# Kernel tuning notes

Hardware: AMD Instinct MI355X
Metric: run time of the kernel (lower is better)

## Reference

```python
import jax, jax.numpy as jnp
import numpy as np
import math

D_MODEL = 1024
NUM_HEADS = 16
D_K = D_MODEL // NUM_HEADS  # 64
THETA = 10000.0
B, S = 2, 2048


def setup_inputs() -> dict:
    key = jax.random.key(0)
    kx, kq, kk, kv, ko = jax.random.split(key, 5)
    sigma = (2.0 / (D_MODEL + D_MODEL)) ** 0.5
    return {
        "x": jax.random.normal(kx, (B, S, D_MODEL), dtype=jnp.float32),
        "Wq": jax.random.normal(kq, (D_MODEL, D_MODEL), dtype=jnp.float32) * sigma,
        "Wk": jax.random.normal(kk, (D_MODEL, D_MODEL), dtype=jnp.float32) * sigma,
        "Wv": jax.random.normal(kv, (D_MODEL, D_MODEL), dtype=jnp.float32) * sigma,
        "Wo": jax.random.normal(ko, (D_MODEL, D_MODEL), dtype=jnp.float32) * sigma,
        "token_positions": jnp.arange(S, dtype=jnp.int32),
    }


def _rope(x, token_positions):
    # x: [..., seq, d_k]; rotate interleaved even/odd pairs.
    half = x.shape[-1] // 2
    freq = jnp.power(THETA, -jnp.arange(0, x.shape[-1], 2, dtype=jnp.float32) / x.shape[-1])  # [half]
    angles = token_positions[:, None].astype(jnp.float32) * freq[None, :]  # [seq, half]
    cos, sin = jnp.cos(angles), jnp.sin(angles)
    x1 = x[..., 0::2]
    x2 = x[..., 1::2]
    out = jnp.stack([x1 * cos - x2 * sin, x1 * sin + x2 * cos], axis=-1)  # [..., seq, half, 2]
    return out.reshape(x.shape)


def reference(x, Wq, Wk, Wv, Wo, token_positions):
    Bb, Ss, Dm = x.shape
    H, Dk = NUM_HEADS, D_K
    # Linear: y = x @ W.T ; split as (n head) -> heads first
    def heads(y):
        return y.reshape(Bb, Ss, H, Dk).transpose(0, 2, 1, 3)  # [B,H,S,Dk]
    Q = heads(x @ Wq.T)
    K = heads(x @ Wk.T)
    V = heads(x @ Wv.T)
    Q = _rope(Q, token_positions)
    K = _rope(K, token_positions)
    scores = jnp.einsum("bhqd,bhkd->bhqk", Q, K) / math.sqrt(Dk)  # [B,H,S,S]
    causal = jnp.tril(jnp.ones((Ss, Ss), dtype=bool))
    scores = jnp.where(causal, scores, -jnp.inf)
    # original casts to fp64 for softmax; numerically-stable fp32 softmax here
    probs = jax.nn.softmax(scores, axis=-1)
    attn = jnp.einsum("bhqk,bhkd->bhqd", probs, V)  # [B,H,S,Dk]
    attn = attn.transpose(0, 2, 1, 3).reshape(Bb, Ss, Dm)
    return attn @ Wo.T
```

## Files before the change

### kernel.cpp

```cpp
#include <hip/hip_runtime.h>
#include <hip/hip_bf16.h>
#include <math.h>

typedef __bf16 bf16_t;
typedef __attribute__((ext_vector_type(8))) __bf16 bf16x8;
typedef __attribute__((ext_vector_type(4))) __bf16 bf16x4;
typedef __attribute__((ext_vector_type(4))) float f32x4;

#define B_DIM 2
#define S_DIM 2048
#define H_DIM 16
#define DK 64
#define DM 1024
#define KDIM 1024

#define MFMA(a, b, c) __builtin_amdgcn_mfma_f32_16x16x32_bf16((a), (b), (c), 0, 0, 0)

__device__ __forceinline__ void gload_lds16(const bf16_t* g, bf16_t* l) {
    __builtin_amdgcn_global_load_lds(
        (const __attribute__((address_space(1))) void*)g,
        (__attribute__((address_space(3))) void*)l, 16, 0, 0);
}

__global__ void cvt_all(const float* __restrict__ x,
                        const float* __restrict__ wq, const float* __restrict__ wk,
                        const float* __restrict__ wv, const float* __restrict__ wo,
                        bf16_t* __restrict__ xb,
                        bf16_t* __restrict__ wqb, bf16_t* __restrict__ wkb,
                        bf16_t* __restrict__ wvb, bf16_t* __restrict__ wob) {
    const long NX = (long)B_DIM * S_DIM * DM;
    const long i = ((long)blockIdx.x * 256 + threadIdx.x) * 4;
    const float* s; bf16_t* d; long off;
    if (i < NX) { s = x; d = xb; off = i; }
    else {
        const long j = i - NX;
        const int wsel = (int)(j >> 20);
        off = j & ((1L << 20) - 1);
        switch (wsel) {
            case 0: s = wq; d = wqb; break;
            case 1: s = wk; d = wkb; break;
            case 2: s = wv; d = wvb; break;
            default: s = wo; d = wob; break;
        }
    }
    float4 v = *reinterpret_cast<const float4*>(s + off);
    bf16x4 o;
    o[0] = (__bf16)v.x; o[1] = (__bf16)v.y; o[2] = (__bf16)v.z; o[3] = (__bf16)v.w;
    *reinterpret_cast<bf16x4*>(d + off) = o;
}

template <int MODE>
__global__ __launch_bounds__(256)
void gemm_bt(const bf16_t* __restrict__ A,
             const bf16_t* __restrict__ B0,
             const bf16_t* __restrict__ B1,
             const bf16_t* __restrict__ B2,
             bf16_t* __restrict__ outQ,
             bf16_t* __restrict__ outK,
             bf16_t* __restrict__ outVt,
             float* __restrict__ outF,
             const int* __restrict__ pos) {
    constexpr int CP = 136;
    constexpr int SELEMS = (MODE == 0) ? (128 * CP) : 16384;
    __shared__ bf16_t smem[SELEMS];
    bf16_t* As = smem;
    bf16_t* Bs = smem + 8192;
    bf16_t* Cs = smem;

    const int t = threadIdx.x;
    const int z = blockIdx.z;
    const bf16_t* Bm = (MODE == 0) ? (z == 0 ? B0 : (z == 1 ? B1 : B2)) : B0;

    const int m0 = blockIdx.x * 128;
    const int n0 = blockIdx.y * 128;
    const int lane = t & 63;
    const int w = t >> 6;
    const int wr = w >> 1;
    const int wc = w & 1;

    f32x4 acc[4][4] = {};

    const bf16_t* Ag = A + (size_t)m0 * KDIM;
    const bf16_t* Bg = Bm + (size_t)n0 * KDIM;

    const int rr = lane & 15;
    const int ko = (lane >> 4) * 8;

    int rI[4], cI[4];
#pragma unroll
    for (int c = 0; c < 4; ++c) {
        const int i = t + c * 256;
        rI[c] = i >> 3;
        cI[c] = ((i & 7) ^ (rI[c] & 7)) * 8;
    }

    for (int k0 = 0; k0 < KDIM; k0 += 64) {
#pragma unroll
        for (int c = 0; c < 4; ++c) {
            const int i = t + c * 256;
            gload_lds16(Ag + (size_t)rI[c] * KDIM + k0 + cI[c], &As[i * 8]);
        }
#pragma unroll
        for (int c = 0; c < 4; ++c) {
            const int i = t + c * 256;
            gload_lds16(Bg + (size_t)rI[c] * KDIM + k0 + cI[c], &Bs[i * 8]);
        }
        __syncthreads();

        bf16x8 af[2][4], bfr[2][4];
#pragma unroll
        for (int kk = 0; kk < 2; ++kk) {
#pragma unroll
            for (int m = 0; m < 4; ++m) {
                const int r = wr * 64 + m * 16 + rr;
                af[kk][m] = *reinterpret_cast<const bf16x8*>(
                    &As[r * 64 + ((kk * 32 + ko) ^ ((r & 7) * 8))]);
            }
#pragma unroll
            for (int n = 0; n < 4; ++n) {
                const int r = wc * 64 + n * 16 + rr;
                bfr[kk][n] = *reinterpret_cast<const bf16x8*>(
                    &Bs[r * 64 + ((kk * 32 + ko) ^ ((r & 7) * 8))]);
            }
        }
        __builtin_amdgcn_s_setprio(1);
#pragma unroll
        for (int kk = 0; kk < 2; ++kk)
#pragma unroll
            for (int m = 0; m < 4; ++m)
#pragma unroll
                for (int n = 0; n < 4; ++n)
                    acc[m][n] = MFMA(af[kk][m], bfr[kk][n], acc[m][n]);
        __builtin_amdgcn_s_setprio(0);
        __syncthreads();
    }

    const int rlb = wr * 64 + (lane >> 4) * 4;
    const int clb = wc * 64 + (lane & 15);

    if (MODE == 0) {
        if (z < 2) {
#pragma unroll
            for (int m = 0; m < 4; ++m)
#pragma unroll
                for (int n = 0; n < 4; ++n)
#pragma unroll
                    for (int j = 0; j < 4; ++j)
                        Cs[(rlb + m * 16 + j) * CP + clb + n * 16] = (__bf16)acc[m][n][j];
            __syncthreads();

            bf16_t* dst = (z == 0) ? outQ : outK;
            const int dch = t & 7;
            const int srow = t >> 3;
            float fr[4];
#pragma unroll
            for (int i = 0; i < 4; ++i)
                fr[i] = exp2f((float)(dch * 4 + i) * -0.4152410118609203f);
#pragma unroll
            for (int p = 0; p < 4; ++p) {
                const int s_loc = p * 32 + srow;
                const int gm = m0 + s_loc;
                const int bb = gm >> 11, sg = gm & (S_DIM - 1);
                const float pv = (float)pos[sg];
                float csv[4], snv[4];
#pragma unroll
                for (int i = 0; i < 4; ++i) {
                    const float a = pv * fr[i];
                    csv[i] = cosf(a); snv[i] = sinf(a);
                }
#pragma unroll
                for (int hc = 0; hc < 2; ++hc) {
                    const bf16x8 vv = *reinterpret_cast<const bf16x8*>(
                        &Cs[s_loc * CP + hc * 64 + dch * 8]);
                    bf16x8 ov;
#pragma unroll
                    for (int i = 0; i < 4; ++i) {
                        const float v0 = (float)vv[2 * i], v1 = (float)vv[2 * i + 1];
                        ov[2 * i]     = (__bf16)(v0 * csv[i] - v1 * snv[i]);
                        ov[2 * i + 1] = (__bf16)(v0 * snv[i] + v1 * csv[i]);
                    }
                    const int h = (n0 >> 6) + hc;
                    *reinterpret_cast<bf16x8*>(
                        &dst[((size_t)(bb * H_DIM + h) * S_DIM + sg) * 64 + dch * 8]) = ov;
                }
            }
        } else {
#pragma unroll
            for (int m = 0; m < 4; ++m)
#pragma unroll
                for (int n = 0; n < 4; ++n) {
                    const int cl = clb + n * 16;
                    bf16x4 v4;
#pragma unroll
                    for (int j = 0; j < 4; ++j) v4[j] = (__bf16)acc[m][n][j];
                    *reinterpret_cast<bf16x4*>(&Cs[cl * CP + rlb + m * 16]) = v4;
                }
            __syncthreads();

            const int cl = t >> 1, sh = t & 1;
            const int cg = n0 + cl, h = cg >> 6, d = cg & 63;
            const int bb = m0 >> 11, s0g = m0 & (S_DIM - 1);
            bf16_t* vdst = &outVt[((size_t)(bb * H_DIM + h) * DK + d) * S_DIM + s0g + sh * 64];
#pragma unroll
            for (int i = 0; i < 8; ++i)
                *reinterpret_cast<bf16x8*>(&vdst[i * 8]) =
                    *reinterpret_cast<const bf16x8*>(&Cs[cl * CP + sh * 64 + i * 8]);
        }
    } else {
        const int rbase = m0 + rlb;
        const int cbase = n0 + clb;
#pragma unroll
        for (int m = 0; m < 4; ++m)
#pragma unroll
            for (int n = 0; n < 4; ++n)
#pragma unroll
                for (int j = 0; j < 4; ++j)
                    outF[(size_t)(rbase + m * 16 + j) * DM + cbase + n * 16] = acc[m][n][j];
    }
}

__global__ __launch_bounds__(256)
void attn_kernel(const bf16_t* __restrict__ Q, const bf16_t* __restrict__ Kg,
                 const bf16_t* __restrict__ Vt, bf16_t* __restrict__ O) {
    constexpr int PSTR = 72;
    __shared__ bf16_t Ks[2][64 * 64];
    __shared__ bf16_t Vs[2][64 * 64];
    __shared__ bf16_t P_lds[4][2][16 * PSTR];

    const int t = threadIdx.x;
    const int lane = t & 63;
    const int w = t >> 6;
    const int bh = blockIdx.x >> 4;
    const int qi = blockIdx.x & 15;
    const int qbH = 31 - qi, qbL = qi;
    const int q0H = qbH * 64 + w * 16;
    const int q0L = qbL * 64 + w * 16;
    const int b = bh >> 4, h = bh & 15;
    const int rr = lane & 15;
    const int hi = lane >> 4;

    const bf16_t* Kbh = Kg + (size_t)bh * S_DIM * DK;
    const bf16_t* Vbh = Vt + (size_t)bh * DK * S_DIM;
    bf16_t* PwH = P_lds[w][0];
    bf16_t* PwL = P_lds[w][1];

    const int i0 = t, i1 = t + 256;
    const int r0 = i0 >> 3, c0 = ((i0 & 7) ^ (r0 & 7)) * 8;
    const int r1 = i1 >> 3, c1 = ((i1 & 7) ^ (r1 & 7)) * 8;

    const float QSCALE = 0.18033688011112042f;
    const bf16_t* QpH = Q + ((size_t)bh * S_DIM + q0H) * DK;
    const bf16_t* QpL = Q + ((size_t)bh * S_DIM + q0L) * DK;
    bf16x8 qfH[2], qfL[2];
    qfH[0] = *reinterpret_cast<const bf16x8*>(&QpH[rr * DK + hi * 8]);
    qfH[1] = *reinterpret_cast<const bf16x8*>(&QpH[rr * DK + 32 + hi * 8]);
    qfL[0] = *reinterpret_cast<const bf16x8*>(&QpL[rr * DK + hi * 8]);
    qfL[1] = *reinterpret_cast<const bf16x8*>(&QpL[rr * DK + 32 + hi * 8]);
#pragma unroll
    for (int i = 0; i < 8; ++i) {
        qfH[0][i] = (__bf16)((float)qfH[0][i] * QSCALE);
        qfH[1][i] = (__bf16)((float)qfH[1][i] * QSCALE);
        qfL[0][i] = (__bf16)((float)qfL[0][i] * QSCALE);
        qfL[1][i] = (__bf16)((float)qfL[1][i] * QSCALE);
    }

    bf16x8 ones;
#pragma unroll
    for (int i = 0; i < 8; ++i) ones[i] = (__bf16)1.0f;

    f32x4 oH[4] = {}, oL[4] = {};
    f32x4 laH = {}, laL = {};
    float mH = -INFINITY, mL = -INFINITY;

    const int ntH = qbH + 1;

    gload_lds16(Kbh + (size_t)r0 * DK + c0, &Ks[0][i0 * 8]);
    gload_lds16(Kbh + (size_t)r1 * DK + c1, &Ks[0][i1 * 8]);
    gload_lds16(Vbh + (size_t)r0 * S_DIM + c0, &Vs[0][i0 * 8]);
    gload_lds16(Vbh + (size_t)r1 * S_DIM + c1, &Vs[0][i1 * 8]);
    __syncthreads();

    for (int tt = 0; tt < ntH; ++tt) {
        const int cur = tt & 1;
        const int kv0 = tt * 64;
        const bool doL = (tt <= qbL);

        if (tt + 1 < ntH) {
            const int kv1 = kv0 + 64;
            bf16_t* Kn = Ks[cur ^ 1];
            bf16_t* Vn = Vs[cur ^ 1];
            gload_lds16(Kbh + (size_t)(kv1 + r0) * DK + c0, &Kn[i0 * 8]);
            gload_lds16(Kbh + (size_t)(kv1 + r1) * DK + c1, &Kn[i1 * 8]);
            gload_lds16(Vbh + (size_t)r0 * S_DIM + kv1 + c0, &Vn[i0 * 8]);
            gload_lds16(Vbh + (size_t)r1 * S_DIM + kv1 + c1, &Vn[i1 * 8]);
        }
        const bf16_t* Kc = Ks[cur];
        const bf16_t* Vc = Vs[cur];

        f32x4 sH[4] = {}, sL[4] = {};
        __builtin_amdgcn_s_setprio(1);
#pragma unroll
        for (int t16 = 0; t16 < 4; ++t16) {
            const int r = t16 * 16 + rr;
            const int sw = (r & 7) * 8;
            bf16x8 kf0 = *reinterpret_cast<const bf16x8*>(&Kc[r * 64 + ((hi * 8) ^ sw)]);
            bf16x8 kf1 = *reinterpret_cast<const bf16x8*>(&Kc[r * 64 + ((32 + hi * 8) ^ sw)]);
            sH[t16] = MFMA(kf0, qfH[0], sH[t16]);
            sH[t16] = MFMA(kf1, qfH[1], sH[t16]);
            if (doL) {
                sL[t16] = MFMA(kf0, qfL[0], sL[t16]);
                sL[t16] = MFMA(kf1, qfL[1], sL[t16]);
            }
        }
        __builtin_amdgcn_s_setprio(0);

        if (tt == qbH) {
            const int qg = q0H + rr;
#pragma unroll
            for (int t16 = 0; t16 < 4; ++t16)
#pragma unroll
                for (int j = 0; j < 4; ++j)
                    if (kv0 + t16 * 16 + hi * 4 + j > qg) sH[t16][j] = -INFINITY;
        }
        if (tt == qbL) {
            const int qg = q0L + rr;
#pragma unroll
            for (int t16 = 0; t16 < 4; ++t16)
#pragma unroll
                for (int j = 0; j < 4; ++j)
                    if (kv0 + t16 * 16 + hi * 4 + j > qg) sL[t16][j] = -INFINITY;
        }

        {
            f32x4 mv = sH[0];
#pragma unroll
            for (int t16 = 1; t16 < 4; ++t16) {
                mv[0] = fmaxf(mv[0], sH[t16][0]); mv[1] = fmaxf(mv[1], sH[t16][1]);
                mv[2] = fmaxf(mv[2], sH[t16][2]); mv[3] = fmaxf(mv[3], sH[t16][3]);
            }
            const float mloc = fmaxf(fmaxf(mv[0], mv[1]), fmaxf(mv[2], mv[3]));
            if (__any(mloc - mH > 8.0f)) {
                float mf = fmaxf(mloc, __shfl_xor(mloc, 16));
                mf = fmaxf(mf, __shfl_xor(mf, 32));
                const float mnew = fmaxf(mH, mf);
                const float scale = exp2f(mH - mnew);
#pragma unroll
                for (int i = 0; i < 4; ++i) laH[i] *= scale;
#pragma unroll
                for (int db = 0; db < 4; ++db)
#pragma unroll
                    for (int j = 0; j < 4; ++j) oH[db][j] *= scale;
                mH = mnew;
            }
#pragma unroll
            for (int t16 = 0; t16 < 4; ++t16) {
                bf16x4 pb;
#pragma unroll
                for (int j = 0; j < 4; ++j) pb[j] = (__bf16)exp2f(sH[t16][j] - mH);
                *reinterpret_cast<bf16x4*>(&PwH[rr * PSTR + t16 * 16 + hi * 4]) = pb;
            }
        }
        if (doL) {
            f32x4 mv = sL[0];
#pragma unroll
            for (int t16 = 1; t16 < 4; ++t16) {
                mv[0] = fmaxf(mv[0], sL[t16][0]); mv[1] = fmaxf(mv[1], sL[t16][1]);
                mv[2] = fmaxf(mv[2], sL[t16][2]); mv[3] = fmaxf(mv[3], sL[t16][3]);
            }
            const float mloc = fmaxf(fmaxf(mv[0], mv[1]), fmaxf(mv[2], mv[3]));
            if (__any(mloc - mL > 8.0f)) {
                float mf = fmaxf(mloc, __shfl_xor(mloc, 16));
                mf = fmaxf(mf, __shfl_xor(mf, 32));
                const float mnew = fmaxf(mL, mf);
                const float scale = exp2f(mL - mnew);
#pragma unroll
                for (int i = 0; i < 4; ++i) laL[i] *= scale;
#pragma unroll
                for (int db = 0; db < 4; ++db)
#pragma unroll
                    for (int j = 0; j < 4; ++j) oL[db][j] *= scale;
                mL = mnew;
            }
#pragma unroll
            for (int t16 = 0; t16 < 4; ++t16) {
                bf16x4 pb;
#pragma unroll
                for (int j = 0; j < 4; ++j) pb[j] = (__bf16)exp2f(sL[t16][j] - mL);
                *reinterpret_cast<bf16x4*>(&PwL[rr * PSTR + t16 * 16 + hi * 4]) = pb;
            }
        }

        bf16x8 pH0 = *reinterpret_cast<const bf16x8*>(&PwH[rr * PSTR + hi * 8]);
        bf16x8 pH1 = *reinterpret_cast<const bf16x8*>(&PwH[rr * PSTR + 32 + hi * 8]);
        bf16x8 pL0, pL1;
        if (doL) {
            pL0 = *reinterpret_cast<const bf16x8*>(&PwL[rr * PSTR + hi * 8]);
            pL1 = *reinterpret_cast<const bf16x8*>(&PwL[rr * PSTR + 32 + hi * 8]);
        }
        __builtin_amdgcn_s_setprio(1);
        laH = MFMA(ones, pH0, laH);
        laH = MFMA(ones, pH1, laH);
        if (doL) {
            laL = MFMA(ones, pL0, laL);
            laL = MFMA(ones, pL1, laL);
        }
#pragma unroll
        for (int db = 0; db < 4; ++db) {
            const int vr = db * 16 + rr;
            const int sw = (vr & 7) * 8;
            bf16x8 vf0 = *reinterpret_cast<const bf16x8*>(&Vc[vr * 64 + ((hi * 8) ^ sw)]);
            bf16x8 vf1 = *reinterpret_cast<const bf16x8*>(&Vc[vr * 64 + ((32 + hi * 8) ^ sw)]);
            oH[db] = MFMA(vf0, pH0, oH[db]);
            oH[db] = MFMA(vf1, pH1, oH[db]);
            if (doL) {
                oL[db] = MFMA(vf0, pL0, oL[db]);
                oL[db] = MFMA(vf1, pL1, oL[db]);
            }
        }
        __builtin_amdgcn_s_setprio(0);

        __syncthreads();
    }

    {
        const float linv = 1.0f / laH[0];
#pragma unroll
        for (int db = 0; db < 4; ++db) {
            bf16x4 ov;
#pragma unroll
            for (int j = 0; j < 4; ++j) ov[j] = (__bf16)(oH[db][j] * linv);
            *reinterpret_cast<bf16x4*>(
                &O[((size_t)(b * S_DIM + q0H + rr)) * DM + h * DK + db * 16 + hi * 4]) = ov;
        }
    }
    {
        const float linv = 1.0f / laL[0];
#pragma unroll
        for (int db = 0; db < 4; ++db) {
            bf16x4 ov;
#pragma unroll
            for (int j = 0; j < 4; ++j) ov[j] = (__bf16)(oL[db][j] * linv);
            *reinterpret_cast<bf16x4*>(
                &O[((size_t)(b * S_DIM + q0L + rr)) * DM + h * DK + db * 16 + hi * 4]) = ov;
        }
    }
}

extern "C" void kernel_launch(void* const* d_in, const int* in_sizes, int n_in,
                              void* d_out, int out_size, void* d_ws, size_t ws_size,
                              hipStream_t stream) {
    const float* x  = (const float*)d_in[0];
    const float* Wq = (const float*)d_in[1];
    const float* Wk = (const float*)d_in[2];
    const float* Wv = (const float*)d_in[3];
    const float* Wo = (const float*)d_in[4];
    const int* pos  = (const int*)d_in[5];
    float* out = (float*)d_out;

    char* ws = (char*)d_ws;
    bf16_t* xb  = (bf16_t*)(ws);
    bf16_t* Wqb = (bf16_t*)(ws + (8u << 20));
    bf16_t* Wkb = (bf16_t*)(ws + (10u << 20));
    bf16_t* Wvb = (bf16_t*)(ws + (12u << 20));
    bf16_t* Wob = (bf16_t*)(ws + (14u << 20));
    bf16_t* Qb  = (bf16_t*)(ws + (16u << 20));
    bf16_t* Kb  = (bf16_t*)(ws + (24u << 20));
    bf16_t* Vtb = (bf16_t*)(ws + (32u << 20));
    bf16_t* Ab  = (bf16_t*)(ws);

    const int NX = B_DIM * S_DIM * DM;
    const int NW = DM * DM;
    const int NTOT = NX + 4 * NW;

    cvt_all<<<NTOT / 1024, 256, 0, stream>>>(x, Wq, Wk, Wv, Wo,
                                             xb, Wqb, Wkb, Wvb, Wob);

    gemm_bt<0><<<dim3(32, 8, 3), 256, 0, stream>>>(xb, Wqb, Wkb, Wvb,
                                                   Qb, Kb, Vtb, nullptr, pos);

    attn_kernel<<<B_DIM * H_DIM * 16, 256, 0, stream>>>(Qb, Kb, Vtb, Ab);

    gemm_bt<1><<<dim3(32, 8, 1), 256, 0, stream>>>(Ab, Wob, nullptr, nullptr,
                                                   nullptr, nullptr, nullptr, out, pos);
}
```

Baseline: 129.8 us.

## Split paired high/low query blocks across separate waves in 512-thread attention blocks

Each attention block now runs 8 waves: waves 0-3 handle the high causal query block and waves 4-7 handle the low one, sharing the same K/V tiles in LDS. Before, each of 4 waves processed both query blocks. Each wave now keeps one set of accumulators, which cuts register pressure and allows more waves per CU for latency hiding. The trade-off is that waves on the low block sit idle at the barriers once their causal range ends, and each K/V tile is now loaded by 512 threads instead of 256.

```diff
diff --git a/kernel.cpp b/kernel.cpp
--- a/kernel.cpp
+++ b/kernel.cpp
@@ -219,13 +219,13 @@
     }
 }
 
-__global__ __launch_bounds__(256)
+__global__ __launch_bounds__(512, 4)
 void attn_kernel(const bf16_t* __restrict__ Q, const bf16_t* __restrict__ Kg,
                  const bf16_t* __restrict__ Vt, bf16_t* __restrict__ O) {
     constexpr int PSTR = 72;
     __shared__ bf16_t Ks[2][64 * 64];
     __shared__ bf16_t Vs[2][64 * 64];
-    __shared__ bf16_t P_lds[4][2][16 * PSTR];
+    __shared__ bf16_t P_lds[8][16 * PSTR];
 
     const int t = threadIdx.x;
     const int lane = t & 63;
@@ -233,216 +233,134 @@
     const int bh = blockIdx.x >> 4;
     const int qi = blockIdx.x & 15;
     const int qbH = 31 - qi, qbL = qi;
-    const int q0H = qbH * 64 + w * 16;
-    const int q0L = qbL * 64 + w * 16;
+    const int qbC = (w < 4) ? qbH : qbL;
+    const int q0 = qbC * 64 + (w & 3) * 16;
     const int b = bh >> 4, h = bh & 15;
     const int rr = lane & 15;
     const int hi = lane >> 4;
 
     const bf16_t* Kbh = Kg + (size_t)bh * S_DIM * DK;
     const bf16_t* Vbh = Vt + (size_t)bh * DK * S_DIM;
-    bf16_t* PwH = P_lds[w][0];
-    bf16_t* PwL = P_lds[w][1];
-
-    const int i0 = t, i1 = t + 256;
-    const int r0 = i0 >> 3, c0 = ((i0 & 7) ^ (r0 & 7)) * 8;
-    const int r1 = i1 >> 3, c1 = ((i1 & 7) ^ (r1 & 7)) * 8;
+    bf16_t* Pw = P_lds[w];
+
+    const int r0 = t >> 3, c0 = ((t & 7) ^ (r0 & 7)) * 8;
 
     const float QSCALE = 0.18033688011112042f;
-    const bf16_t* QpH = Q + ((size_t)bh * S_DIM + q0H) * DK;
-    const bf16_t* QpL = Q + ((size_t)bh * S_DIM + q0L) * DK;
-    bf16x8 qfH[2], qfL[2];
-    qfH[0] = *reinterpret_cast<const bf16x8*>(&QpH[rr * DK + hi * 8]);
-    qfH[1] = *reinterpret_cast<const bf16x8*>(&QpH[rr * DK + 32 + hi * 8]);
-    qfL[0] = *reinterpret_cast<const bf16x8*>(&QpL[rr * DK + hi * 8]);
-    qfL[1] = *reinterpret_cast<const bf16x8*>(&QpL[rr * DK + 32 + hi * 8]);
+    const bf16_t* Qp = Q + ((size_t)bh * S_DIM + q0) * DK;
+    bf16x8 qf[2];
+    qf[0] = *reinterpret_cast<const bf16x8*>(&Qp[rr * DK + hi * 8]);
+    qf[1] = *reinterpret_cast<const bf16x8*>(&Qp[rr * DK + 32 + hi * 8]);
 #pragma unroll
     for (int i = 0; i < 8; ++i) {
-        qfH[0][i] = (__bf16)((float)qfH[0][i] * QSCALE);
-        qfH[1][i] = (__bf16)((float)qfH[1][i] * QSCALE);
-        qfL[0][i] = (__bf16)((float)qfL[0][i] * QSCALE);
-        qfL[1][i] = (__bf16)((float)qfL[1][i] * QSCALE);
+        qf[0][i] = (__bf16)((float)qf[0][i] * QSCALE);
+        qf[1][i] = (__bf16)((float)qf[1][i] * QSCALE);
     }
 
     bf16x8 ones;
 #pragma unroll
     for (int i = 0; i < 8; ++i) ones[i] = (__bf16)1.0f;
 
-    f32x4 oH[4] = {}, oL[4] = {};
-    f32x4 laH = {}, laL = {};
-    float mH = -INFINITY, mL = -INFINITY;
+    f32x4 o[4] = {};
+    f32x4 la = {};
+    float m = -INFINITY;
 
     const int ntH = qbH + 1;
 
-    gload_lds16(Kbh + (size_t)r0 * DK + c0, &Ks[0][i0 * 8]);
-    gload_lds16(Kbh + (size_t)r1 * DK + c1, &Ks[0][i1 * 8]);
-    gload_lds16(Vbh + (size_t)r0 * S_DIM + c0, &Vs[0][i0 * 8]);
-    gload_lds16(Vbh + (size_t)r1 * S_DIM + c1, &Vs[0][i1 * 8]);
+    gload_lds16(Kbh + (size_t)r0 * DK + c0, &Ks[0][t * 8]);
+    gload_lds16(Vbh + (size_t)r0 * S_DIM + c0, &Vs[0][t * 8]);
     __syncthreads();
 
     for (int tt = 0; tt < ntH; ++tt) {
         const int cur = tt & 1;
         const int kv0 = tt * 64;
-        const bool doL = (tt <= qbL);
 
         if (tt + 1 < ntH) {
             const int kv1 = kv0 + 64;
-            bf16_t* Kn = Ks[cur ^ 1];
-            bf16_t* Vn = Vs[cur ^ 1];
-            gload_lds16(Kbh + (size_t)(kv1 + r0) * DK + c0, &Kn[i0 * 8]);
-            gload_lds16(Kbh + (size_t)(kv1 + r1) * DK + c1, &Kn[i1 * 8]);
-            gload_lds16(Vbh + (size_t)r0 * S_DIM + kv1 + c0, &Vn[i0 * 8]);
-            gload_lds16(Vbh + (size_t)r1 * S_DIM + kv1 + c1, &Vn[i1 * 8]);
+            gload_lds16(Kbh + (size_t)(kv1 + r0) * DK + c0, &Ks[cur ^ 1][t * 8]);
+            gload_lds16(Vbh + (size_t)r0 * S_DIM + kv1 + c0, &Vs[cur ^ 1][t * 8]);
         }
         const bf16_t* Kc = Ks[cur];
         const bf16_t* Vc = Vs[cur];
 
-        f32x4 sH[4] = {}, sL[4] = {};
-        __builtin_amdgcn_s_setprio(1);
-#pragma unroll
-        for (int t16 = 0; t16 < 4; ++t16) {
-            const int r = t16 * 16 + rr;
-            const int sw = (r & 7) * 8;
-            bf16x8 kf0 = *reinterpret_cast<const bf16x8*>(&Kc[r * 64 + ((hi * 8) ^ sw)]);
-            bf16x8 kf1 = *reinterpret_cast<const bf16x8*>(&Kc[r * 64 + ((32 + hi * 8) ^ sw)]);
-            sH[t16] = MFMA(kf0, qfH[0], sH[t16]);
-            sH[t16] = MFMA(kf1, qfH[1], sH[t16]);
-            if (doL) {
-                sL[t16] = MFMA(kf0, qfL[0], sL[t16]);
-                sL[t16] = MFMA(kf1, qfL[1], sL[t16]);
-            }
-        }
-        __builtin_amdgcn_s_setprio(0);
-
-        if (tt == qbH) {
-            const int qg = q0H + rr;
-#pragma unroll
-            for (int t16 = 0; t16 < 4; ++t16)
-#pragma unroll
-                for (int j = 0; j < 4; ++j)
-                    if (kv0 + t16 * 16 + hi * 4 + j > qg) sH[t16][j] = -INFINITY;
-        }
-        if (tt == qbL) {
-            const int qg = q0L + rr;
-#pragma unroll
-            for (int t16 = 0; t16 < 4; ++t16)
-#pragma unroll
-                for (int j = 0; j < 4; ++j)
-                    if (kv0 + t16 * 16 + hi * 4 + j > qg) sL[t16][j] = -INFINITY;
-        }
-
-        {
-            f32x4 mv = sH[0];
+        if (tt <= qbC) {
+            f32x4 s[4] = {};
+            __builtin_amdgcn_s_setprio(1);
+#pragma unroll
+            for (int t16 = 0; t16 < 4; ++t16) {
+                const int r = t16 * 16 + rr;
+                const int sw = (r & 7) * 8;
+                bf16x8 kf0 = *reinterpret_cast<const bf16x8*>(&Kc[r * 64 + ((hi * 8) ^ sw)]);
+                bf16x8 kf1 = *reinterpret_cast<const bf16x8*>(&Kc[r * 64 + ((32 + hi * 8) ^ sw)]);
+                s[t16] = MFMA(kf0, qf[0], s[t16]);
+                s[t16] = MFMA(kf1, qf[1], s[t16]);
+            }
+            __builtin_amdgcn_s_setprio(0);
+
+            if (tt == qbC) {
+                const int qg = q0 + rr;
+#pragma unroll
+                for (int t16 = 0; t16 < 4; ++t16)
+#pragma unroll
+                    for (int j = 0; j < 4; ++j)
+                        if (kv0 + t16 * 16 + hi * 4 + j > qg) s[t16][j] = -INFINITY;
+            }
+
+            f32x4 mv = s[0];
 #pragma unroll
             for (int t16 = 1; t16 < 4; ++t16) {
-                mv[0] = fmaxf(mv[0], sH[t16][0]); mv[1] = fmaxf(mv[1], sH[t16][1]);
-                mv[2] = fmaxf(mv[2], sH[t16][2]); mv[3] = fmaxf(mv[3], sH[t16][3]);
+                mv[0] = fmaxf(mv[0], s[t16][0]); mv[1] = fmaxf(mv[1], s[t16][1]);
+                mv[2] = fmaxf(mv[2], s[t16][2]); mv[3] = fmaxf(mv[3], s[t16][3]);
             }
             const float mloc = fmaxf(fmaxf(mv[0], mv[1]), fmaxf(mv[2], mv[3]));
-            if (__any(mloc - mH > 8.0f)) {
+            if (__any(mloc - m > 8.0f)) {
                 float mf = fmaxf(mloc, __shfl_xor(mloc, 16));
                 mf = fmaxf(mf, __shfl_xor(mf, 32));
-                const float mnew = fmaxf(mH, mf);
-                const float scale = exp2f(mH - mnew);
-#pragma unroll
-                for (int i = 0; i < 4; ++i) laH[i] *= scale;
+                const float mnew = fmaxf(m, mf);
+                const float scale = exp2f(m - mnew);
+#pragma unroll
+                for (int i = 0; i < 4; ++i) la[i] *= scale;
 #pragma unroll
                 for (int db = 0; db < 4; ++db)
 #pragma unroll
-                    for (int j = 0; j < 4; ++j) oH[db][j] *= scale;
-                mH = mnew;
+                    for (int j = 0; j < 4; ++j) o[db][j] *= scale;
+                m = mnew;
             }
 #pragma unroll
             for (int t16 = 0; t16 < 4; ++t16) {
                 bf16x4 pb;
 #pragma unroll
-                for (int j = 0; j < 4; ++j) pb[j] = (__bf16)exp2f(sH[t16][j] - mH);
-                *reinterpret_cast<bf16x4*>(&PwH[rr * PSTR + t16 * 16 + hi * 4]) = pb;
-            }
-        }
-        if (doL) {
-            f32x4 mv = sL[0];
-#pragma unroll
-            for (int t16 = 1; t16 < 4; ++t16) {
-                mv[0] = fmaxf(mv[0], sL[t16][0]); mv[1] = fmaxf(mv[1], sL[t16][1]);
-                mv[2] = fmaxf(mv[2], sL[t16][2]); mv[3] = fmaxf(mv[3], sL[t16][3]);
-            }
-            const float mloc = fmaxf(fmaxf(mv[0], mv[1]), fmaxf(mv[2], mv[3]));
-            if (__any(mloc - mL > 8.0f)) {
-                float mf = fmaxf(mloc, __shfl_xor(mloc, 16));
-                mf = fmaxf(mf, __shfl_xor(mf, 32));
-                const float mnew = fmaxf(mL, mf);
-                const float scale = exp2f(mL - mnew);
-#pragma unroll
-                for (int i = 0; i < 4; ++i) laL[i] *= scale;
-#pragma unroll
-                for (int db = 0; db < 4; ++db)
-#pragma unroll
-                    for (int j = 0; j < 4; ++j) oL[db][j] *= scale;
-                mL = mnew;
-            }
-#pragma unroll
-            for (int t16 = 0; t16 < 4; ++t16) {
-                bf16x4 pb;
-#pragma unroll
-                for (int j = 0; j < 4; ++j) pb[j] = (__bf16)exp2f(sL[t16][j] - mL);
-                *reinterpret_cast<bf16x4*>(&PwL[rr * PSTR + t16 * 16 + hi * 4]) = pb;
-            }
-        }
-
-        bf16x8 pH0 = *reinterpret_cast<const bf16x8*>(&PwH[rr * PSTR + hi * 8]);
-        bf16x8 pH1 = *reinterpret_cast<const bf16x8*>(&PwH[rr * PSTR + 32 + hi * 8]);
-        bf16x8 pL0, pL1;
-        if (doL) {
-            pL0 = *reinterpret_cast<const bf16x8*>(&PwL[rr * PSTR + hi * 8]);
-            pL1 = *reinterpret_cast<const bf16x8*>(&PwL[rr * PSTR + 32 + hi * 8]);
-        }
-        __builtin_amdgcn_s_setprio(1);
-        laH = MFMA(ones, pH0, laH);
-        laH = MFMA(ones, pH1, laH);
-        if (doL) {
-            laL = MFMA(ones, pL0, laL);
-            laL = MFMA(ones, pL1, laL);
-        }
-#pragma unroll
-        for (int db = 0; db < 4; ++db) {
-            const int vr = db * 16 + rr;
-            const int sw = (vr & 7) * 8;
-            bf16x8 vf0 = *reinterpret_cast<const bf16x8*>(&Vc[vr * 64 + ((hi * 8) ^ sw)]);
-            bf16x8 vf1 = *reinterpret_cast<const bf16x8*>(&Vc[vr * 64 + ((32 + hi * 8) ^ sw)]);
-            oH[db] = MFMA(vf0, pH0, oH[db]);
-            oH[db] = MFMA(vf1, pH1, oH[db]);
-            if (doL) {
-                oL[db] = MFMA(vf0, pL0, oL[db]);
-                oL[db] = MFMA(vf1, pL1, oL[db]);
-            }
-        }
-        __builtin_amdgcn_s_setprio(0);
+                for (int j = 0; j < 4; ++j) pb[j] = (__bf16)exp2f(s[t16][j] - m);
+                *reinterpret_cast<bf16x4*>(&Pw[rr * PSTR + t16 * 16 + hi * 4]) = pb;
+            }
+
+            bf16x8 pf0 = *reinterpret_cast<const bf16x8*>(&Pw[rr * PSTR + hi * 8]);
+            bf16x8 pf1 = *reinterpret_cast<const bf16x8*>(&Pw[rr * PSTR + 32 + hi * 8]);
+            __builtin_amdgcn_s_setprio(1);
+            la = MFMA(ones, pf0, la);
+            la = MFMA(ones, pf1, la);
+#pragma unroll
+            for (int db = 0; db < 4; ++db) {
+                const int vr = db * 16 + rr;
+                const int sw = (vr & 7) * 8;
+                bf16x8 vf0 = *reinterpret_cast<const bf16x8*>(&Vc[vr * 64 + ((hi * 8) ^ sw)]);
+                bf16x8 vf1 = *reinterpret_cast<const bf16x8*>(&Vc[vr * 64 + ((32 + hi * 8) ^ sw)]);
+                o[db] = MFMA(vf0, pf0, o[db]);
+                o[db] = MFMA(vf1, pf1, o[db]);
+            }
+            __builtin_amdgcn_s_setprio(0);
+        }
 
         __syncthreads();
     }
 
-    {
-        const float linv = 1.0f / laH[0];
-#pragma unroll
-        for (int db = 0; db < 4; ++db) {
-            bf16x4 ov;
-#pragma unroll
-            for (int j = 0; j < 4; ++j) ov[j] = (__bf16)(oH[db][j] * linv);
-            *reinterpret_cast<bf16x4*>(
-                &O[((size_t)(b * S_DIM + q0H + rr)) * DM + h * DK + db * 16 + hi * 4]) = ov;
-        }
-    }
-    {
-        const float linv = 1.0f / laL[0];
-#pragma unroll
-        for (int db = 0; db < 4; ++db) {
-            bf16x4 ov;
-#pragma unroll
-            for (int j = 0; j < 4; ++j) ov[j] = (__bf16)(oL[db][j] * linv);
-            *reinterpret_cast<bf16x4*>(
-                &O[((size_t)(b * S_DIM + q0L + rr)) * DM + h * DK + db * 16 + hi * 4]) = ov;
-        }
+    const float linv = 1.0f / la[0];
+#pragma unroll
+    for (int db = 0; db < 4; ++db) {
+        bf16x4 ov;
+#pragma unroll
+        for (int j = 0; j < 4; ++j) ov[j] = (__bf16)(o[db][j] * linv);
+        *reinterpret_cast<bf16x4*>(
+            &O[((size_t)(b * S_DIM + q0 + rr)) * DM + h * DK + db * 16 + hi * 4]) = ov;
     }
 }
 
@@ -478,7 +396,7 @@
     gemm_bt<0><<<dim3(32, 8, 3), 256, 0, stream>>>(xb, Wqb, Wkb, Wvb,
                                                    Qb, Kb, Vtb, nullptr, pos);
 
-    attn_kernel<<<B_DIM * H_DIM * 16, 256, 0, stream>>>(Qb, Kb, Vtb, Ab);
+    attn_kernel<<<B_DIM * H_DIM * 16, 512, 0, stream>>>(Qb, Kb, Vtb, Ab);
 
     gemm_bt<1><<<dim3(32, 8, 1), 256, 0, stream>>>(Ab, Wob, nullptr, nullptr,
                                                    nullptr, nullptr, nullptr, out, pos);
```

After: 113.9 us. -12.2%, faster.
